# Optimization experiments

Hardware: AMD Instinct MI355X
Metric: run time of the kernel (lower is better)

## Reference

```python
import jax, jax.numpy as jnp
import numpy as np

WH, WW = 7, 7
N = WH * WW
DIM = 256
HEADS = 8
HEAD_DIM = DIM // HEADS
SCALE = HEAD_DIM ** -0.5


def _relative_position_index():
    coords = np.stack(np.meshgrid(np.arange(WH), np.arange(WW), indexing='ij'))  # [2,Wh,Ww]
    cf = coords.reshape(2, -1)                      # [2,N]
    rel = cf[:, :, None] - cf[:, None, :]           # [2,N,N]
    rel = rel.transpose(1, 2, 0)                    # [N,N,2]
    rel[..., 0] += WH - 1
    rel[..., 1] += WW - 1
    rel[..., 0] *= 2 * WW - 1
    return rel.sum(-1)                              # [N,N] in [0, (2Wh-1)(2Ww-1))

_REL_IDX = jnp.asarray(_relative_position_index())


def setup_inputs() -> dict:
    key = jax.random.key(0)
    ks = jax.random.split(key, 6)
    B_ = 8192
    return {
        'x': jax.random.normal(ks[0], (B_, N, DIM), dtype=jnp.float32),
        'qkv_w': jax.random.normal(ks[1], (3 * DIM, DIM), dtype=jnp.float32) * 0.02,
        'qkv_b': jax.random.normal(ks[2], (3 * DIM,), dtype=jnp.float32) * 0.02,
        'proj_w': jax.random.normal(ks[3], (DIM, DIM), dtype=jnp.float32) * 0.02,
        'proj_b': jax.random.normal(ks[4], (DIM,), dtype=jnp.float32) * 0.02,
        'bias_table': jax.random.normal(ks[5], ((2 * WH - 1) * (2 * WW - 1), HEADS), dtype=jnp.float32) * 0.02,
    }


def reference(x, qkv_w, qkv_b, proj_w, proj_b, bias_table):
    B_, n, C = x.shape
    # QKV projection -> [3, B_, H, N, hd]
    qkv = (x @ qkv_w.T + qkv_b).reshape(B_, n, 3, HEADS, HEAD_DIM)
    qkv = jnp.transpose(qkv, (2, 0, 3, 1, 4))
    q, k, v = qkv[0], qkv[1], qkv[2]
    # Gathered relative position bias: [H, N, N]
    bias = bias_table[_REL_IDX.reshape(-1)].reshape(n, n, HEADS).transpose(2, 0, 1)
    # Scaled dot-product attention with additive bias
    attn = jnp.einsum('bhnd,bhmd->bhnm', q, k) * SCALE + bias[None]
    attn = jax.nn.softmax(attn, axis=-1)
    out = jnp.einsum('bhnm,bhmd->bhnd', attn, v)
    out = jnp.transpose(out, (0, 2, 1, 3)).reshape(B_, n, C)
    return out @ proj_w.T + proj_b
```

## Files before the change

kernel.cpp:

```cpp
#include <hip/hip_runtime.h>
#include <hip/hip_bf16.h>
#include <stdint.h>

#define NTOK 49
#define SCALE 0.17677669529663687f

typedef __attribute__((ext_vector_type(8))) short bf16x8;
typedef __attribute__((ext_vector_type(4))) float f32x4;

__device__ __forceinline__ unsigned short f2bf(float f) {
    union { float f; unsigned int u; } v; v.f = f;
    unsigned int r = v.u + 0x7FFFu + ((v.u >> 16) & 1u);
    return (unsigned short)(r >> 16);
}

__device__ __forceinline__ uint32_t pkbf(float lo, float hi) {
    __hip_bfloat162 h = __float22bfloat162_rn(float2{lo, hi});
    union { __hip_bfloat162 h; uint32_t u; } c; c.h = h;
    return c.u;
}

__global__ void prep_kernel(const float* __restrict__ qkv_w,
                            const float* __restrict__ proj_w,
                            const float* __restrict__ bias_table,
                            const float* __restrict__ qkv_b,
                            unsigned short* __restrict__ w_qkv,
                            unsigned short* __restrict__ w_proj,
                            float* __restrict__ bias_p,
                            float* __restrict__ sbias) {
    const int total = 196608 + 65536 + 32768 + 768;
    for (int i = blockIdx.x * blockDim.x + threadIdx.x; i < total;
         i += gridDim.x * blockDim.x) {
        if (i < 196608) {
            float s = (i < 65536) ? SCALE : 1.0f;
            w_qkv[i] = f2bf(qkv_w[i] * s);
        } else if (i < 262144) {
            w_proj[i - 196608] = f2bf(proj_w[i - 196608]);
        } else if (i < 294912) {
            int idx = i - 262144;
            int hh = idx >> 12;
            int j  = (idx >> 6) & 63;
            int ii = idx & 63;
            float v;
            if (j >= NTOK)       v = -1e30f;
            else if (ii >= NTOK) v = 0.0f;
            else {
                int rel = (ii / 7 - j / 7 + 6) * 13 + (ii % 7 - j % 7 + 6);
                v = bias_table[rel * 8 + hh];
            }
            bias_p[hh * 4096 + (j >> 2) * 256 + ii * 4 + (j & 3)] = v;
        } else {
            int r = i - 294912;
            sbias[r] = qkv_b[r] * (r < 256 ? SCALE : 1.0f);
        }
    }
}

__global__ __launch_bounds__(512, 4) void wattn_kernel(
    const float* __restrict__ x,
    const unsigned short* __restrict__ w_qkv,
    const unsigned short* __restrict__ w_proj,
    const float* __restrict__ bias_p,
    const float* __restrict__ sbias,
    const float* __restrict__ proj_b,
    float* __restrict__ out)
{
    extern __shared__ char smem[];
    unsigned short* sX = (unsigned short*)smem;
    unsigned short* scrBase = sX + 64 * 264;

    const int tid  = threadIdx.x;
    const int wv   = tid >> 6;
    const int lane = tid & 63;
    const int l16  = lane & 15;
    const int g    = lane >> 4;
    const int lk   = g * 8;

    unsigned short* scr = scrBase + wv * (64 * 36);
    const int b = blockIdx.x;
    const int h = wv;
    const f32x4 fz = {0.f, 0.f, 0.f, 0.f};

    const float* xb = x + (size_t)b * (NTOK * 256);
    for (int it = tid * 4; it < NTOK * 256; it += 512 * 4) {
        float4 v = *(const float4*)(xb + it);
        int r = it >> 8, c = it & 255;
        uint2 u = make_uint2(pkbf(v.x, v.y), pkbf(v.z, v.w));
        *(uint2*)(sX + r * 264 + c) = u;
    }
    for (int it = tid * 4; it < 15 * 256; it += 512 * 4) {
        int r = 49 + (it >> 8), c = it & 255;
        *(uint2*)(sX + r * 264 + c) = make_uint2(0, 0);
    }
    __syncthreads();

    bf16x8 qf[4], kf[4], vf[2][2];

    {
        f32x4 acc[2][4];
        #pragma unroll
        for (int mt = 0; mt < 2; ++mt)
            #pragma unroll
            for (int nt = 0; nt < 4; ++nt) acc[mt][nt] = fz;

        #pragma unroll 2
        for (int kb = 0; kb < 8; ++kb) {
            bf16x8 bx[4];
            #pragma unroll
            for (int nt = 0; nt < 4; ++nt)
                bx[nt] = *(const bf16x8*)(sX + (nt * 16 + l16) * 264 + kb * 32 + lk);
            #pragma unroll
            for (int mt = 0; mt < 2; ++mt) {
                bf16x8 aw = *(const bf16x8*)(w_qkv + (h * 32 + mt * 16 + l16) * 256 + kb * 32 + lk);
                #pragma unroll
                for (int nt = 0; nt < 4; ++nt)
                    acc[mt][nt] = __builtin_amdgcn_mfma_f32_16x16x32_bf16(
                        aw, bx[nt], acc[mt][nt], 0, 0, 0);
            }
        }
        float4 bq0 = *(const float4*)(sbias + h * 32 + 4 * g);
        float4 bq1 = *(const float4*)(sbias + h * 32 + 16 + 4 * g);
        #pragma unroll
        for (int nt = 0; nt < 4; ++nt) {
            acc[0][nt][0] += bq0.x; acc[0][nt][1] += bq0.y;
            acc[0][nt][2] += bq0.z; acc[0][nt][3] += bq0.w;
            acc[1][nt][0] += bq1.x; acc[1][nt][1] += bq1.y;
            acc[1][nt][2] += bq1.z; acc[1][nt][3] += bq1.w;
        }
        #pragma unroll
        for (int nt = 0; nt < 4; ++nt)
            #pragma unroll
            for (int mt = 0; mt < 2; ++mt) {
                uint2 d = make_uint2(pkbf(acc[mt][nt][0], acc[mt][nt][1]),
                                     pkbf(acc[mt][nt][2], acc[mt][nt][3]));
                *(uint2*)(scr + (nt * 16 + l16) * 36 + mt * 16 + 4 * g) = d;
            }
        #pragma unroll
        for (int nt = 0; nt < 4; ++nt)
            qf[nt] = *(const bf16x8*)(scr + (nt * 16 + l16) * 36 + lk);
    }

    {
        f32x4 acc[2][4];
        #pragma unroll
        for (int mt = 0; mt < 2; ++mt)
            #pragma unroll
            for (int nt = 0; nt < 4; ++nt) acc[mt][nt] = fz;

        #pragma unroll 2
        for (int kb = 0; kb < 8; ++kb) {
            bf16x8 bx[4];
            #pragma unroll
            for (int nt = 0; nt < 4; ++nt)
                bx[nt] = *(const bf16x8*)(sX + (nt * 16 + l16) * 264 + kb * 32 + lk);
            #pragma unroll
            for (int mt = 0; mt < 2; ++mt) {
                bf16x8 aw = *(const bf16x8*)(w_qkv + (256 + h * 32 + mt * 16 + l16) * 256 + kb * 32 + lk);
                #pragma unroll
                for (int nt = 0; nt < 4; ++nt)
                    acc[mt][nt] = __builtin_amdgcn_mfma_f32_16x16x32_bf16(
                        aw, bx[nt], acc[mt][nt], 0, 0, 0);
            }
        }
        #pragma unroll
        for (int nt = 0; nt < 4; ++nt)
            #pragma unroll
            for (int mt = 0; mt < 2; ++mt) {
                uint2 d = make_uint2(pkbf(acc[mt][nt][0], acc[mt][nt][1]),
                                     pkbf(acc[mt][nt][2], acc[mt][nt][3]));
                *(uint2*)(scr + (nt * 16 + l16) * 36 + mt * 16 + 4 * g) = d;
            }
        #pragma unroll
        for (int nt = 0; nt < 4; ++nt)
            kf[nt] = *(const bf16x8*)(scr + (nt * 16 + l16) * 36 + lk);
    }

    {
        f32x4 acc[4][2];
        #pragma unroll
        for (int rt = 0; rt < 4; ++rt) { acc[rt][0] = fz; acc[rt][1] = fz; }

        #pragma unroll 2
        for (int kb = 0; kb < 8; ++kb) {
            bf16x8 ax[4];
            #pragma unroll
            for (int rt = 0; rt < 4; ++rt)
                ax[rt] = *(const bf16x8*)(sX + (rt * 16 + l16) * 264 + kb * 32 + lk);
            #pragma unroll
            for (int ct = 0; ct < 2; ++ct) {
                bf16x8 bw = *(const bf16x8*)(w_qkv + (512 + h * 32 + ct * 16 + l16) * 256 + kb * 32 + lk);
                #pragma unroll
                for (int rt = 0; rt < 4; ++rt)
                    acc[rt][ct] = __builtin_amdgcn_mfma_f32_16x16x32_bf16(
                        ax[rt], bw, acc[rt][ct], 0, 0, 0);
            }
        }
        #pragma unroll
        for (int rt = 0; rt < 4; ++rt)
            #pragma unroll
            for (int ct = 0; ct < 2; ++ct) {
                uint2 d = make_uint2(pkbf(acc[rt][ct][0], acc[rt][ct][1]),
                                     pkbf(acc[rt][ct][2], acc[rt][ct][3]));
                *(uint2*)(scr + ((rt >> 1) * 32 + ct * 16 + l16) * 36 + (rt & 1) * 16 + 4 * g) = d;
            }
        #pragma unroll
        for (int dm = 0; dm < 2; ++dm)
            #pragma unroll
            for (int kk = 0; kk < 2; ++kk)
                vf[dm][kk] = *(const bf16x8*)(scr + (kk * 32 + dm * 16 + l16) * 36 + lk);
    }

    const float* bp_h = bias_p + h * 4096;
    float4 bv0 = *(const float4*)(sbias + 512 + h * 32 + 4 * g);
    float4 bv1 = *(const float4*)(sbias + 512 + h * 32 + 16 + 4 * g);

    uint2 o_st[2][2][2];

    #pragma unroll
    for (int hf = 0; hf < 2; ++hf) {
        f32x4 s[4][2];
        #pragma unroll
        for (int tr = 0; tr < 4; ++tr)
            #pragma unroll
            for (int tl = 0; tl < 2; ++tl) {
                const int i = (hf * 2 + tl) * 16 + l16;
                s[tr][tl] = *(const f32x4*)(bp_h + (tr * 4 + g) * 256 + i * 4);
            }
        __builtin_amdgcn_s_setprio(1);
        #pragma unroll
        for (int tr = 0; tr < 4; ++tr)
            #pragma unroll
            for (int tl = 0; tl < 2; ++tl)
                s[tr][tl] = __builtin_amdgcn_mfma_f32_16x16x32_bf16(
                    kf[tr], qf[hf * 2 + tl], s[tr][tl], 0, 0, 0);
        __builtin_amdgcn_s_setprio(0);

        float inv[2];
        #pragma unroll
        for (int tl = 0; tl < 2; ++tl) {
            float s4[4];
            #pragma unroll
            for (int tr = 0; tr < 4; ++tr) {
                float e0 = __expf(s[tr][tl][0]);
                float e1 = __expf(s[tr][tl][1]);
                float e2 = __expf(s[tr][tl][2]);
                float e3 = __expf(s[tr][tl][3]);
                s[tr][tl][0] = e0; s[tr][tl][1] = e1;
                s[tr][tl][2] = e2; s[tr][tl][3] = e3;
                s4[tr] = (e0 + e1) + (e2 + e3);
            }
            float sum = (s4[0] + s4[1]) + (s4[2] + s4[3]);
            sum += __shfl_xor(sum, 16);
            sum += __shfl_xor(sum, 32);
            inv[tl] = 1.0f / sum;
        }

        #pragma unroll
        for (int tr = 0; tr < 4; ++tr)
            #pragma unroll
            for (int tl = 0; tl < 2; ++tl) {
                uint2 d = make_uint2(pkbf(s[tr][tl][0], s[tr][tl][1]),
                                     pkbf(s[tr][tl][2], s[tr][tl][3]));
                *(uint2*)(scr + ((tr >> 1) * 32 + tl * 16 + l16) * 36 + (tr & 1) * 16 + 4 * g) = d;
            }
        bf16x8 pf[2][2];
        #pragma unroll
        for (int tl = 0; tl < 2; ++tl)
            #pragma unroll
            for (int kk = 0; kk < 2; ++kk)
                pf[tl][kk] = *(const bf16x8*)(scr + (kk * 32 + tl * 16 + l16) * 36 + lk);

        f32x4 o[2][2];
        #pragma unroll
        for (int dm = 0; dm < 2; ++dm) { o[dm][0] = fz; o[dm][1] = fz; }
        __builtin_amdgcn_s_setprio(1);
        #pragma unroll
        for (int dm = 0; dm < 2; ++dm)
            #pragma unroll
            for (int tl = 0; tl < 2; ++tl)
                #pragma unroll
                for (int kk = 0; kk < 2; ++kk)
                    o[dm][tl] = __builtin_amdgcn_mfma_f32_16x16x32_bf16(
                        vf[dm][kk], pf[tl][kk], o[dm][tl], 0, 0, 0);
        __builtin_amdgcn_s_setprio(0);

        #pragma unroll
        for (int dm = 0; dm < 2; ++dm) {
            const float4 bv = dm ? bv1 : bv0;
            #pragma unroll
            for (int tl = 0; tl < 2; ++tl) {
                const float iv = inv[tl];
                float r0 = o[dm][tl][0] * iv + bv.x;
                float r1 = o[dm][tl][1] * iv + bv.y;
                float r2 = o[dm][tl][2] * iv + bv.z;
                float r3 = o[dm][tl][3] * iv + bv.w;
                o_st[hf][dm][tl] = make_uint2(pkbf(r0, r1), pkbf(r2, r3));
            }
        }
    }

    __syncthreads();

    #pragma unroll
    for (int hf = 0; hf < 2; ++hf)
        #pragma unroll
        for (int dm = 0; dm < 2; ++dm)
            #pragma unroll
            for (int tl = 0; tl < 2; ++tl)
                *(uint2*)(sX + ((hf * 2 + tl) * 16 + l16) * 264 + h * 32 + dm * 16 + 4 * g)
                    = o_st[hf][dm][tl];
    __syncthreads();

    {
        f32x4 acc[4][2];
        #pragma unroll
        for (int rt = 0; rt < 4; ++rt) { acc[rt][0] = fz; acc[rt][1] = fz; }

        const int colbase = wv * 32;
        #pragma unroll 2
        for (int kb = 0; kb < 8; ++kb) {
            bf16x8 a[4];
            #pragma unroll
            for (int rt = 0; rt < 4; ++rt)
                a[rt] = *(const bf16x8*)(sX + (rt * 16 + l16) * 264 + kb * 32 + lk);
            #pragma unroll
            for (int c = 0; c < 2; ++c) {
                bf16x8 bw = *(const bf16x8*)(w_proj + (colbase + c * 16 + l16) * 256 + kb * 32 + lk);
                #pragma unroll
                for (int rt = 0; rt < 4; ++rt)
                    acc[rt][c] = __builtin_amdgcn_mfma_f32_16x16x32_bf16(
                        a[rt], bw, acc[rt][c], 0, 0, 0);
            }
        }
        float* ob = out + (size_t)b * (NTOK * 256);
        #pragma unroll
        for (int c = 0; c < 2; ++c) {
            const int col = colbase + c * 16 + l16;
            const float pb = proj_b[col];
            #pragma unroll
            for (int rt = 0; rt < 4; ++rt)
                #pragma unroll
                for (int r = 0; r < 4; ++r) {
                    const int row = rt * 16 + 4 * g + r;
                    if (row < NTOK) ob[row * 256 + col] = acc[rt][c][r] + pb;
                }
        }
    }
}

extern "C" void kernel_launch(void* const* d_in, const int* in_sizes, int n_in,
                              void* d_out, int out_size, void* d_ws, size_t ws_size,
                              hipStream_t stream) {
    const float* x          = (const float*)d_in[0];
    const float* qkv_w      = (const float*)d_in[1];
    const float* qkv_b      = (const float*)d_in[2];
    const float* proj_w     = (const float*)d_in[3];
    const float* proj_b     = (const float*)d_in[4];
    const float* bias_table = (const float*)d_in[5];

    unsigned short* w_qkv  = (unsigned short*)d_ws;
    unsigned short* w_proj = w_qkv + 196608;
    float*          bias_p = (float*)(w_proj + 65536);
    float*          sbias  = bias_p + 32768;

    prep_kernel<<<288, 256, 0, stream>>>(qkv_w, proj_w, bias_table, qkv_b,
                                         w_qkv, w_proj, bias_p, sbias);

    const int SMEM = (64 * 264 + 8 * 64 * 36) * 2;
    hipFuncSetAttribute(reinterpret_cast<const void*>(wattn_kernel),
                        hipFuncAttributeMaxDynamicSharedMemorySize, SMEM);

    wattn_kernel<<<8192, 512, SMEM, stream>>>(x, w_qkv, w_proj, bias_p, sbias,
                                              proj_b, (float*)d_out);
}
```

Before: 645.1 us.

## Fuse Q and K projections into one pass, use exp2 softmax, unroll loads

Q and K projections are now computed in a single loop with a 4x4 accumulator tile, so X fragments are read from shared memory once instead of twice. LOG2E is folded into the Q weights, Q bias and relative position bias, which lets the softmax use the hardware exp2 directly. The X staging loop is fully unrolled with fixed trip counts, and the output store drops its per-element row bounds check. The larger accumulator raises register pressure, which may hurt occupancy under launch_bounds(512,4).

```diff
diff --git a/kernel.cpp b/kernel.cpp
--- a/kernel.cpp
+++ b/kernel.cpp
@@ -4,6 +4,7 @@
 
 #define NTOK 49
 #define SCALE 0.17677669529663687f
+#define LOG2E 1.4426950408889634f
 
 typedef __attribute__((ext_vector_type(8))) short bf16x8;
 typedef __attribute__((ext_vector_type(4))) float f32x4;
@@ -32,7 +33,7 @@
     for (int i = blockIdx.x * blockDim.x + threadIdx.x; i < total;
          i += gridDim.x * blockDim.x) {
         if (i < 196608) {
-            float s = (i < 65536) ? SCALE : 1.0f;
+            float s = (i < 65536) ? SCALE * LOG2E : 1.0f;
             w_qkv[i] = f2bf(qkv_w[i] * s);
         } else if (i < 262144) {
             w_proj[i - 196608] = f2bf(proj_w[i - 196608]);
@@ -48,10 +49,10 @@
                 int rel = (ii / 7 - j / 7 + 6) * 13 + (ii % 7 - j % 7 + 6);
                 v = bias_table[rel * 8 + hh];
             }
-            bias_p[hh * 4096 + (j >> 2) * 256 + ii * 4 + (j & 3)] = v;
+            bias_p[hh * 4096 + (j >> 2) * 256 + ii * 4 + (j & 3)] = v * LOG2E;
         } else {
             int r = i - 294912;
-            sbias[r] = qkv_b[r] * (r < 256 ? SCALE : 1.0f);
+            sbias[r] = qkv_b[r] * (r < 256 ? SCALE * LOG2E : 1.0f);
         }
     }
 }
@@ -82,24 +83,34 @@
     const f32x4 fz = {0.f, 0.f, 0.f, 0.f};
 
     const float* xb = x + (size_t)b * (NTOK * 256);
-    for (int it = tid * 4; it < NTOK * 256; it += 512 * 4) {
-        float4 v = *(const float4*)(xb + it);
-        int r = it >> 8, c = it & 255;
-        uint2 u = make_uint2(pkbf(v.x, v.y), pkbf(v.z, v.w));
-        *(uint2*)(sX + r * 264 + c) = u;
-    }
-    for (int it = tid * 4; it < 15 * 256; it += 512 * 4) {
-        int r = 49 + (it >> 8), c = it & 255;
-        *(uint2*)(sX + r * 264 + c) = make_uint2(0, 0);
+    #pragma unroll
+    for (int it = 0; it < 6; ++it) {
+        const int idx = tid * 4 + it * 2048;
+        float4 v = *(const float4*)(xb + idx);
+        int r = idx >> 8, c = idx & 255;
+        *(uint2*)(sX + r * 264 + c) = make_uint2(pkbf(v.x, v.y), pkbf(v.z, v.w));
+    }
+    if (tid < 64) {
+        const int idx = tid * 4 + 12288;
+        float4 v = *(const float4*)(xb + idx);
+        int r = idx >> 8, c = idx & 255;
+        *(uint2*)(sX + r * 264 + c) = make_uint2(pkbf(v.x, v.y), pkbf(v.z, v.w));
+    }
+    {
+        const int i0 = tid * 4;
+        *(uint2*)(sX + (49 + (i0 >> 8)) * 264 + (i0 & 255)) = make_uint2(0, 0);
+        const int i1 = i0 + 2048;
+        if (i1 < 3840)
+            *(uint2*)(sX + (49 + (i1 >> 8)) * 264 + (i1 & 255)) = make_uint2(0, 0);
     }
     __syncthreads();
 
     bf16x8 qf[4], kf[4], vf[2][2];
 
     {
-        f32x4 acc[2][4];
-        #pragma unroll
-        for (int mt = 0; mt < 2; ++mt)
+        f32x4 acc[4][4];
+        #pragma unroll
+        for (int mt = 0; mt < 4; ++mt)
             #pragma unroll
             for (int nt = 0; nt < 4; ++nt) acc[mt][nt] = fz;
 
@@ -110,8 +121,10 @@
             for (int nt = 0; nt < 4; ++nt)
                 bx[nt] = *(const bf16x8*)(sX + (nt * 16 + l16) * 264 + kb * 32 + lk);
             #pragma unroll
-            for (int mt = 0; mt < 2; ++mt) {
-                bf16x8 aw = *(const bf16x8*)(w_qkv + (h * 32 + mt * 16 + l16) * 256 + kb * 32 + lk);
+            for (int mt = 0; mt < 4; ++mt) {
+                const int wrow = (mt < 2) ? (h * 32 + mt * 16 + l16)
+                                          : (256 + h * 32 + (mt - 2) * 16 + l16);
+                bf16x8 aw = *(const bf16x8*)(w_qkv + wrow * 256 + kb * 32 + lk);
                 #pragma unroll
                 for (int nt = 0; nt < 4; ++nt)
                     acc[mt][nt] = __builtin_amdgcn_mfma_f32_16x16x32_bf16(
@@ -138,37 +151,13 @@
         #pragma unroll
         for (int nt = 0; nt < 4; ++nt)
             qf[nt] = *(const bf16x8*)(scr + (nt * 16 + l16) * 36 + lk);
-    }
-
-    {
-        f32x4 acc[2][4];
-        #pragma unroll
-        for (int mt = 0; mt < 2; ++mt)
-            #pragma unroll
-            for (int nt = 0; nt < 4; ++nt) acc[mt][nt] = fz;
-
-        #pragma unroll 2
-        for (int kb = 0; kb < 8; ++kb) {
-            bf16x8 bx[4];
-            #pragma unroll
-            for (int nt = 0; nt < 4; ++nt)
-                bx[nt] = *(const bf16x8*)(sX + (nt * 16 + l16) * 264 + kb * 32 + lk);
-            #pragma unroll
-            for (int mt = 0; mt < 2; ++mt) {
-                bf16x8 aw = *(const bf16x8*)(w_qkv + (256 + h * 32 + mt * 16 + l16) * 256 + kb * 32 + lk);
-                #pragma unroll
-                for (int nt = 0; nt < 4; ++nt)
-                    acc[mt][nt] = __builtin_amdgcn_mfma_f32_16x16x32_bf16(
-                        aw, bx[nt], acc[mt][nt], 0, 0, 0);
-            }
-        }
         #pragma unroll
         for (int nt = 0; nt < 4; ++nt)
             #pragma unroll
-            for (int mt = 0; mt < 2; ++mt) {
+            for (int mt = 2; mt < 4; ++mt) {
                 uint2 d = make_uint2(pkbf(acc[mt][nt][0], acc[mt][nt][1]),
                                      pkbf(acc[mt][nt][2], acc[mt][nt][3]));
-                *(uint2*)(scr + (nt * 16 + l16) * 36 + mt * 16 + 4 * g) = d;
+                *(uint2*)(scr + (nt * 16 + l16) * 36 + (mt - 2) * 16 + 4 * g) = d;
             }
         #pragma unroll
         for (int nt = 0; nt < 4; ++nt)
@@ -241,10 +230,10 @@
             float s4[4];
             #pragma unroll
             for (int tr = 0; tr < 4; ++tr) {
-                float e0 = __expf(s[tr][tl][0]);
-                float e1 = __expf(s[tr][tl][1]);
-                float e2 = __expf(s[tr][tl][2]);
-                float e3 = __expf(s[tr][tl][3]);
+                float e0 = __builtin_amdgcn_exp2f(s[tr][tl][0]);
+                float e1 = __builtin_amdgcn_exp2f(s[tr][tl][1]);
+                float e2 = __builtin_amdgcn_exp2f(s[tr][tl][2]);
+                float e3 = __builtin_amdgcn_exp2f(s[tr][tl][3]);
                 s[tr][tl][0] = e0; s[tr][tl][1] = e1;
                 s[tr][tl][2] = e2; s[tr][tl][3] = e3;
                 s4[tr] = (e0 + e1) + (e2 + e3);
@@ -338,12 +327,11 @@
             const int col = colbase + c * 16 + l16;
             const float pb = proj_b[col];
             #pragma unroll
-            for (int rt = 0; rt < 4; ++rt)
-                #pragma unroll
-                for (int r = 0; r < 4; ++r) {
-                    const int row = rt * 16 + 4 * g + r;
-                    if (row < NTOK) ob[row * 256 + col] = acc[rt][c][r] + pb;
-                }
+            for (int rt = 0; rt < 3; ++rt)
+                #pragma unroll
+                for (int r = 0; r < 4; ++r)
+                    ob[(rt * 16 + 4 * g + r) * 256 + col] = acc[rt][c][r] + pb;
+            if (g == 0) ob[48 * 256 + col] = acc[3][c][0] + pb;
         }
     }
 }
```

Result: faster. 604.6 us (median of 2 runs) (-6.3%).
